# Performance work log

Measured on AMD Instinct MI355X. Metric: run time of the kernel, lower is better.

The kernel has to match this reference:

```python
import jax, jax.numpy as jnp
import numpy as np

N = 50000
E = 800000
F_IN = 96
HID = 128
NCLS = 40
EPS = 0.0  # GINConv default eps


def _mlp(h, W1, b1, W2, b2):
    # Linear -> ReLU -> Linear
    h = jax.nn.relu(h @ W1 + b1)
    return h @ W2 + b2


def _gin_conv(x, edge_index, W1, b1, W2, b2):
    src, dst = edge_index[0], edge_index[1]
    # sum-aggregate neighbor features: scatter-add x[src] into dst
    agg = jax.ops.segment_sum(x[src], dst, num_segments=N)
    return _mlp((1.0 + EPS) * x + agg, W1, b1, W2, b2)


def setup_inputs() -> dict:
    key = jax.random.key(0)
    ks = jax.random.split(key, 12)

    def lin(kw, fan_in, fan_out):
        bound = 1.0 / np.sqrt(fan_in)
        k1, k2 = jax.random.split(kw)
        W = jax.random.uniform(k1, (fan_in, fan_out), jnp.float32, -bound, bound)
        b = jax.random.uniform(k2, (fan_out,), jnp.float32, -bound, bound)
        return W, b

    x = jax.random.normal(ks[0], (N, F_IN), jnp.float32)
    edge_index = jax.random.randint(ks[1], (2, E), 0, N, jnp.int64)
    W1a, b1a = lin(ks[2], F_IN, HID)
    W2a, b2a = lin(ks[3], HID, HID)
    W1b, b1b = lin(ks[4], HID, HID)
    W2b, b2b = lin(ks[5], HID, HID)
    Wfc, bfc = lin(ks[6], HID, NCLS)
    return {"x": x, "edge_index": edge_index,
            "W1a": W1a, "b1a": b1a, "W2a": W2a, "b2a": b2a,
            "W1b": W1b, "b1b": b1b, "W2b": W2b, "b2b": b2b,
            "Wfc": Wfc, "bfc": bfc}


def reference(x, edge_index, W1a, b1a, W2a, b2a, W1b, b1b, W2b, b2b, Wfc, bfc):
    h = _gin_conv(x, edge_index, W1a, b1a, W2a, b2a)
    h = jax.nn.relu(h)
    h = _gin_conv(h, edge_index, W1b, b1b, W2b, b2b)
    return h @ Wfc + bfc  # [N, NCLS]
```

## Files before the change

### kernel.cpp

```cpp
#include <hip/hip_runtime.h>

constexpr int N_NODES = 50000;
constexpr int N_EDGES = 800000;
constexpr int F_INPUT = 96;
constexpr int HID = 128;
constexpr int NCLS = 40;
constexpr int REC = 64;
constexpr int ENT = 62;
constexpr int NBIN = 196;
constexpr int CAPB = 4608;

typedef __attribute__((ext_vector_type(8))) short short8;
typedef __attribute__((ext_vector_type(4))) float f32x4;

__device__ __forceinline__ float bf2f(unsigned int u16) {
    unsigned int x = u16 << 16;
    return __builtin_bit_cast(float, x);
}
__device__ __forceinline__ unsigned short f2bf(float f) {
    unsigned int x = __builtin_bit_cast(unsigned int, f);
    x += 0x7fffu + ((x >> 16) & 1u);
    return (unsigned short)(x >> 16);
}

constexpr int PA_R1 = 391;
constexpr int PA_XC = (N_NODES * F_INPUT / 4 + 255) / 256;
constexpr int PA_F0 = PA_R1 + PA_XC;
constexpr int PA_W1 = PA_F0 + 33;
constexpr int PA_W2 = PA_W1 + 48;
constexpr int PA_W3 = PA_W2 + 64;
constexpr int PA_END = PA_W3 + 64;

__global__ __launch_bounds__(256) void prep_all(
    const float* __restrict__ x,
    const float* __restrict__ W1a, const float* __restrict__ W2a,
    const float* __restrict__ W1b, const float* __restrict__ W2b,
    const float* __restrict__ b2b, const float* __restrict__ Wfc,
    const float* __restrict__ bfc, const int* __restrict__ ei,
    unsigned short* __restrict__ W1aT, unsigned short* __restrict__ W2aT,
    unsigned short* __restrict__ W1bT, unsigned short* __restrict__ WcT,
    float* __restrict__ bc, int* __restrict__ binCursor,
    unsigned int* __restrict__ binBuf, unsigned short* __restrict__ xb) {
    const int b = blockIdx.x;
    const int tid = threadIdx.x;
    if (b < PA_R1) {
        __shared__ int cnt[NBIN];
        __shared__ int base[NBIN];
        for (int i = tid; i < NBIN; i += 256) cnt[i] = 0;
        __syncthreads();
        int binq[8], posq[8];
        unsigned int recq[8];
#pragma unroll
        for (int q = 0; q < 8; ++q) {
            int e = b * 2048 + q * 256 + tid;
            binq[q] = -1;
            if (e < N_EDGES) {
                int src = ei[e], dst = ei[N_EDGES + e];
                int bin = dst >> 8;
                binq[q] = bin;
                recq[q] = (unsigned int)(src & 0xffff) | ((unsigned int)(dst & 255) << 16);
                posq[q] = atomicAdd(&cnt[bin], 1);
            }
        }
        __syncthreads();
        for (int i = tid; i < NBIN; i += 256)
            base[i] = (cnt[i] > 0) ? atomicAdd(&binCursor[i], cnt[i]) : 0;
        __syncthreads();
#pragma unroll
        for (int q = 0; q < 8; ++q) {
            if (binq[q] >= 0) {
                int off = base[binq[q]] + posq[q];
                if (off < CAPB) binBuf[(size_t)binq[q] * CAPB + off] = recq[q];
            }
        }
    } else if (b < PA_F0) {
        int e4 = ((b - PA_R1) * 256 + tid) * 4;
        if (e4 < N_NODES * F_INPUT) {
            float4 v = *reinterpret_cast<const float4*>(&x[e4]);
            uint2 o;
            o.x = (unsigned int)f2bf(v.x) | ((unsigned int)f2bf(v.y) << 16);
            o.y = (unsigned int)f2bf(v.z) | ((unsigned int)f2bf(v.w) << 16);
            *reinterpret_cast<uint2*>(&xb[e4]) = o;
        }
    } else if (b < PA_W1) {
        int idx = (b - PA_F0) * 256 + tid;
        if (idx < 64 * 128) {
            int n = idx >> 7, k = idx & 127;
            float s = 0.f;
            if (n < NCLS) {
                for (int j = 0; j < 128; ++j) s += W2b[k * 128 + j] * Wfc[j * NCLS + n];
            }
            WcT[idx] = f2bf(s);
        } else if (idx < 64 * 128 + 64) {
            int n = idx - 64 * 128;
            float s = 0.f;
            if (n < NCLS) {
                s = bfc[n];
                for (int j = 0; j < 128; ++j) s += b2b[j] * Wfc[j * NCLS + n];
            }
            bc[n] = s;
        }
    } else if (b < PA_W2) {
        int idx = (b - PA_W1) * 256 + tid;
        int n = idx / 96, k = idx % 96;
        W1aT[idx] = f2bf(W1a[k * 128 + n]);
    } else if (b < PA_W3) {
        int idx = (b - PA_W2) * 256 + tid;
        int n = idx >> 7, k = idx & 127;
        W2aT[idx] = f2bf(W2a[k * 128 + n]);
    } else {
        int idx = (b - PA_W3) * 256 + tid;
        int n = idx >> 7, k = idx & 127;
        W1bT[idx] = f2bf(W1b[k * 128 + n]);
    }
}

__global__ __launch_bounds__(1024) void radix2(const int* __restrict__ binCursor,
                                               const unsigned int* __restrict__ binBuf,
                                               unsigned short* __restrict__ bucket) {
    __shared__ int lcnt[256];
    const int bin = blockIdx.x;
    const int tid = threadIdx.x;
    for (int i = tid; i < 256; i += 1024) lcnt[i] = 0;
    __syncthreads();
    int n = binCursor[bin];
    if (n > CAPB) n = CAPB;
    for (int i = tid; i < n; i += 1024) {
        unsigned int r = binBuf[(size_t)bin * CAPB + i];
        int low = (int)(r >> 16);
        int pos = atomicAdd(&lcnt[low], 1);
        if (pos < ENT)
            bucket[(size_t)((bin << 8) + low) * REC + 2 + pos] = (unsigned short)(r & 0xffff);
    }
    __syncthreads();
    for (int i = tid; i < 256; i += 1024) {
        int node = (bin << 8) + i;
        if (node < N_NODES) {
            int c = lcnt[i];
            *reinterpret_cast<int*>(&bucket[(size_t)node * REC]) = (c > ENT ? ENT : c);
        }
    }
}

template<int F>
__global__ __launch_bounds__(256) void gather_bf(const unsigned short* __restrict__ X,
                                                 const unsigned short* __restrict__ bucket,
                                                 unsigned short* __restrict__ OUT) {
    const int wave = threadIdx.x >> 6;
    const int lane = threadIdx.x & 63;
    const int node = blockIdx.x * 4 + wave;
    if (node >= N_NODES) return;
    const unsigned short* rec = &bucket[(size_t)node * REC];
    int deg = *reinterpret_cast<const int*>(rec);
    if (deg > ENT) deg = ENT;

    int v = (lane < deg) ? (int)rec[2 + lane] : 0x7fffffff;
#pragma unroll
    for (int k = 2; k <= 64; k <<= 1) {
#pragma unroll
        for (int j = k >> 1; j > 0; j >>= 1) {
            int pv = __shfl_xor(v, j, 64);
            bool keepmin = (((lane & k) == 0) == ((lane & j) == 0));
            v = keepmin ? (pv < v ? pv : v) : (pv > v ? pv : v);
        }
    }

    const int f = lane * 2;
    const bool act = (f < F);
    float a0 = 0.f, a1 = 0.f;
    int j = 0;
    for (; j + 7 < deg; j += 8) {
        int s[8];
        unsigned int vv[8];
#pragma unroll
        for (int q = 0; q < 8; ++q) s[q] = __shfl(v, j + q, 64);
#pragma unroll
        for (int q = 0; q < 8; ++q) {
            if (act) vv[q] = *reinterpret_cast<const unsigned int*>(&X[(size_t)s[q] * F + f]);
        }
        if (act) {
#pragma unroll
            for (int q = 0; q < 8; ++q) {
                a0 += bf2f(vv[q] & 0xffff);
                a1 += bf2f(vv[q] >> 16);
            }
        }
    }
    if (j + 3 < deg) {
        int s[4];
        unsigned int vv[4];
#pragma unroll
        for (int q = 0; q < 4; ++q) s[q] = __shfl(v, j + q, 64);
#pragma unroll
        for (int q = 0; q < 4; ++q) {
            if (act) vv[q] = *reinterpret_cast<const unsigned int*>(&X[(size_t)s[q] * F + f]);
        }
        if (act) {
#pragma unroll
            for (int q = 0; q < 4; ++q) {
                a0 += bf2f(vv[q] & 0xffff);
                a1 += bf2f(vv[q] >> 16);
            }
        }
        j += 4;
    }
    for (; j < deg; ++j) {
        int s = __shfl(v, j, 64);
        if (act) {
            unsigned int vx = *reinterpret_cast<const unsigned int*>(&X[(size_t)s * F + f]);
            a0 += bf2f(vx & 0xffff);
            a1 += bf2f(vx >> 16);
        }
    }
    if (act) {
        unsigned int xv = *reinterpret_cast<const unsigned int*>(&X[(size_t)node * F + f]);
        a0 += bf2f(xv & 0xffff);
        a1 += bf2f(xv >> 16);
        unsigned int o = (unsigned int)f2bf(a0) | ((unsigned int)f2bf(a1) << 16);
        *reinterpret_cast<unsigned int*>(&OUT[(size_t)node * F + f]) = o;
    }
}

template<int K1, int NT2, int NCOUT, bool RELU2, bool BF16_OUT>
__global__ __launch_bounds__(256) void mlp_fused(const unsigned short* __restrict__ A,
                                                 const unsigned short* __restrict__ W1T,
                                                 const float* __restrict__ b1,
                                                 const unsigned short* __restrict__ W2T,
                                                 const float* __restrict__ b2,
                                                 void* __restrict__ Cout, int M) {
    constexpr int KS1 = K1 / 32;
    constexpr int NT1 = 8;
    constexpr int K2 = 128;
    constexpr int KS2 = K2 / 32;
    __shared__ __align__(16) unsigned short sH[4][16][136];

    const int tid = threadIdx.x;
    const int lane = tid & 63;
    const int wv = tid >> 6;
    const int rowbase = blockIdx.x * 64 + wv * 16;
    const int rA = lane & 15;
    const int kg = lane >> 4;

    int r0 = rowbase + rA;
    if (r0 >= M) r0 = M - 1;
    const unsigned short* ap = A + (size_t)r0 * K1 + kg * 8;
    const unsigned short* b1p = W1T + (size_t)rA * K1 + kg * 8;

    f32x4 acc1[NT1] = {};
#pragma unroll
    for (int ks = 0; ks < KS1; ++ks) {
        short8 a = *reinterpret_cast<const short8*>(ap + ks * 32);
#pragma unroll
        for (int nt = 0; nt < NT1; ++nt) {
            short8 b = *reinterpret_cast<const short8*>(b1p + nt * 16 * K1 + ks * 32);
            acc1[nt] = __builtin_amdgcn_mfma_f32_16x16x32_bf16(a, b, acc1[nt], 0, 0, 0);
        }
    }

    const int oc = lane & 15;
    const int orow = (lane >> 4) * 4;
#pragma unroll
    for (int nt = 0; nt < NT1; ++nt) {
        float bz = b1[nt * 16 + oc];
#pragma unroll
        for (int r = 0; r < 4; ++r) {
            float v = fmaxf(acc1[nt][r] + bz, 0.f);
            sH[wv][orow + r][nt * 16 + oc] = f2bf(v);
        }
    }
    __syncthreads();

    const unsigned short* b2p = W2T + (size_t)rA * K2 + kg * 8;
    f32x4 acc2[NT2] = {};
#pragma unroll
    for (int ks = 0; ks < KS2; ++ks) {
        short8 a = *reinterpret_cast<const short8*>(&sH[wv][rA][kg * 8 + ks * 32]);
#pragma unroll
        for (int nt = 0; nt < NT2; ++nt) {
            short8 b = *reinterpret_cast<const short8*>(b2p + nt * 16 * K2 + ks * 32);
            acc2[nt] = __builtin_amdgcn_mfma_f32_16x16x32_bf16(a, b, acc2[nt], 0, 0, 0);
        }
    }

#pragma unroll
    for (int nt = 0; nt < NT2; ++nt) {
        int col = nt * 16 + oc;
        if (col >= NCOUT) continue;
        float bz = b2[col];
#pragma unroll
        for (int r = 0; r < 4; ++r) {
            int row = rowbase + orow + r;
            if (row < M) {
                float v = acc2[nt][r] + bz;
                if (RELU2) v = fmaxf(v, 0.f);
                if (BF16_OUT)
                    ((unsigned short*)Cout)[(size_t)row * NCOUT + col] = f2bf(v);
                else
                    ((float*)Cout)[(size_t)row * NCOUT + col] = v;
            }
        }
    }
}

extern "C" void kernel_launch(void* const* d_in, const int* in_sizes, int n_in,
                              void* d_out, int out_size, void* d_ws, size_t ws_size,
                              hipStream_t stream) {
    const float* x   = (const float*)d_in[0];
    const int*   ei  = (const int*)d_in[1];
    const float* W1a = (const float*)d_in[2];
    const float* b1a = (const float*)d_in[3];
    const float* W2a = (const float*)d_in[4];
    const float* b2a = (const float*)d_in[5];
    const float* W1b = (const float*)d_in[6];
    const float* b1b = (const float*)d_in[7];
    const float* W2b = (const float*)d_in[8];
    const float* b2b = (const float*)d_in[9];
    const float* Wfc = (const float*)d_in[10];
    const float* bfc = (const float*)d_in[11];
    float* out = (float*)d_out;

    char* p = (char*)d_ws;
    auto alloc = [&](size_t bytes) {
        char* r = p;
        p += (bytes + 255) & ~size_t(255);
        return r;
    };
    unsigned short* xb   = (unsigned short*)alloc((size_t)N_NODES * F_INPUT * 2);
    unsigned short* h0   = (unsigned short*)alloc((size_t)N_NODES * F_INPUT * 2);
    unsigned short* t    = (unsigned short*)alloc((size_t)N_NODES * HID * 2);
    unsigned short* g    = (unsigned short*)alloc((size_t)N_NODES * HID * 2);
    unsigned short* W1aT = (unsigned short*)alloc(128 * 96 * 2);
    unsigned short* W2aT = (unsigned short*)alloc(128 * 128 * 2);
    unsigned short* W1bT = (unsigned short*)alloc(128 * 128 * 2);
    unsigned short* WcT  = (unsigned short*)alloc(64 * 128 * 2);
    float* bc            = (float*)alloc(64 * 4);
    int* binCursor       = (int*)alloc(NBIN * 4);
    unsigned int* binBuf = (unsigned int*)alloc((size_t)NBIN * CAPB * 4);
    unsigned short* bucket = (unsigned short*)alloc((size_t)N_NODES * REC * 2);

    const int nb4 = (N_NODES + 3) / 4;
    const int mb = (N_NODES + 63) / 64;

    hipMemsetAsync(binCursor, 0, NBIN * sizeof(int), stream);

    prep_all<<<PA_END, 256, 0, stream>>>(x, W1a, W2a, W1b, W2b, b2b, Wfc, bfc, ei,
                                         W1aT, W2aT, W1bT, WcT, bc, binCursor, binBuf, xb);

    radix2<<<NBIN, 1024, 0, stream>>>(binCursor, binBuf, bucket);

    gather_bf<F_INPUT><<<nb4, 256, 0, stream>>>(xb, bucket, h0);
    mlp_fused<96, 8, 128, true, true><<<mb, 256, 0, stream>>>(h0, W1aT, b1a, W2aT, b2a, t,
                                                              N_NODES);

    gather_bf<HID><<<nb4, 256, 0, stream>>>(t, bucket, g);
    mlp_fused<128, 4, 40, false, false><<<mb, 256, 0, stream>>>(g, W1bT, b1b, WcT, bc, out,
                                                                N_NODES);
}
```

Before: 232.8 us.

## Fuse neighbor gather-aggregation into the MLP kernel via shared memory

Replaces the separate gather_bf and mlp_fused launches with a single gin_fused kernel. Each wave now aggregates neighbor features for its 16 rows in sequence, writing them into a shared-memory tile that feeds the first MFMA GEMM directly. This removes the h0 and g intermediate buffers, their global writes and reads, and two kernel launches. The cost is less gather parallelism: one wave processes 16 nodes one after another, and far fewer waves are launched, so memory latency may be harder to hide. The now-unneeded block barrier is also dropped, since each wave only touches its own shared rows.

```diff
diff --git a/kernel.cpp b/kernel.cpp
--- a/kernel.cpp
+++ b/kernel.cpp
@@ -142,87 +142,9 @@
     }
 }
 
-template<int F>
-__global__ __launch_bounds__(256) void gather_bf(const unsigned short* __restrict__ X,
+template<int K1, int PADA, int NT2, int NCOUT, bool RELU2, bool BF16_OUT>
+__global__ __launch_bounds__(256) void gin_fused(const unsigned short* __restrict__ X,
                                                  const unsigned short* __restrict__ bucket,
-                                                 unsigned short* __restrict__ OUT) {
-    const int wave = threadIdx.x >> 6;
-    const int lane = threadIdx.x & 63;
-    const int node = blockIdx.x * 4 + wave;
-    if (node >= N_NODES) return;
-    const unsigned short* rec = &bucket[(size_t)node * REC];
-    int deg = *reinterpret_cast<const int*>(rec);
-    if (deg > ENT) deg = ENT;
-
-    int v = (lane < deg) ? (int)rec[2 + lane] : 0x7fffffff;
-#pragma unroll
-    for (int k = 2; k <= 64; k <<= 1) {
-#pragma unroll
-        for (int j = k >> 1; j > 0; j >>= 1) {
-            int pv = __shfl_xor(v, j, 64);
-            bool keepmin = (((lane & k) == 0) == ((lane & j) == 0));
-            v = keepmin ? (pv < v ? pv : v) : (pv > v ? pv : v);
-        }
-    }
-
-    const int f = lane * 2;
-    const bool act = (f < F);
-    float a0 = 0.f, a1 = 0.f;
-    int j = 0;
-    for (; j + 7 < deg; j += 8) {
-        int s[8];
-        unsigned int vv[8];
-#pragma unroll
-        for (int q = 0; q < 8; ++q) s[q] = __shfl(v, j + q, 64);
-#pragma unroll
-        for (int q = 0; q < 8; ++q) {
-            if (act) vv[q] = *reinterpret_cast<const unsigned int*>(&X[(size_t)s[q] * F + f]);
-        }
-        if (act) {
-#pragma unroll
-            for (int q = 0; q < 8; ++q) {
-                a0 += bf2f(vv[q] & 0xffff);
-                a1 += bf2f(vv[q] >> 16);
-            }
-        }
-    }
-    if (j + 3 < deg) {
-        int s[4];
-        unsigned int vv[4];
-#pragma unroll
-        for (int q = 0; q < 4; ++q) s[q] = __shfl(v, j + q, 64);
-#pragma unroll
-        for (int q = 0; q < 4; ++q) {
-            if (act) vv[q] = *reinterpret_cast<const unsigned int*>(&X[(size_t)s[q] * F + f]);
-        }
-        if (act) {
-#pragma unroll
-            for (int q = 0; q < 4; ++q) {
-                a0 += bf2f(vv[q] & 0xffff);
-                a1 += bf2f(vv[q] >> 16);
-            }
-        }
-        j += 4;
-    }
-    for (; j < deg; ++j) {
-        int s = __shfl(v, j, 64);
-        if (act) {
-            unsigned int vx = *reinterpret_cast<const unsigned int*>(&X[(size_t)s * F + f]);
-            a0 += bf2f(vx & 0xffff);
-            a1 += bf2f(vx >> 16);
-        }
-    }
-    if (act) {
-        unsigned int xv = *reinterpret_cast<const unsigned int*>(&X[(size_t)node * F + f]);
-        a0 += bf2f(xv & 0xffff);
-        a1 += bf2f(xv >> 16);
-        unsigned int o = (unsigned int)f2bf(a0) | ((unsigned int)f2bf(a1) << 16);
-        *reinterpret_cast<unsigned int*>(&OUT[(size_t)node * F + f]) = o;
-    }
-}
-
-template<int K1, int NT2, int NCOUT, bool RELU2, bool BF16_OUT>
-__global__ __launch_bounds__(256) void mlp_fused(const unsigned short* __restrict__ A,
                                                  const unsigned short* __restrict__ W1T,
                                                  const float* __restrict__ b1,
                                                  const unsigned short* __restrict__ W2T,
@@ -232,24 +154,94 @@
     constexpr int NT1 = 8;
     constexpr int K2 = 128;
     constexpr int KS2 = K2 / 32;
+    __shared__ __align__(16) unsigned short sA[4][16][PADA];
     __shared__ __align__(16) unsigned short sH[4][16][136];
 
     const int tid = threadIdx.x;
     const int lane = tid & 63;
     const int wv = tid >> 6;
     const int rowbase = blockIdx.x * 64 + wv * 16;
+
+    for (int i = 0; i < 16; ++i) {
+        const int node = rowbase + i;
+        if (node >= M) break;
+        const unsigned short* rec = &bucket[(size_t)node * REC];
+        int deg = *reinterpret_cast<const int*>(rec);
+        if (deg > ENT) deg = ENT;
+        int v = (lane < deg) ? (int)rec[2 + lane] : 0x7fffffff;
+#pragma unroll
+        for (int k = 2; k <= 64; k <<= 1) {
+#pragma unroll
+            for (int j = k >> 1; j > 0; j >>= 1) {
+                int pv = __shfl_xor(v, j, 64);
+                bool keepmin = (((lane & k) == 0) == ((lane & j) == 0));
+                v = keepmin ? (pv < v ? pv : v) : (pv > v ? pv : v);
+            }
+        }
+        const int f = lane * 2;
+        const bool act = (f < K1);
+        float a0 = 0.f, a1 = 0.f;
+        int j = 0;
+        for (; j + 7 < deg; j += 8) {
+            int s[8];
+            unsigned int vv[8];
+#pragma unroll
+            for (int q = 0; q < 8; ++q) s[q] = __shfl(v, j + q, 64);
+#pragma unroll
+            for (int q = 0; q < 8; ++q) {
+                if (act) vv[q] = *reinterpret_cast<const unsigned int*>(&X[(size_t)s[q] * K1 + f]);
+            }
+            if (act) {
+#pragma unroll
+                for (int q = 0; q < 8; ++q) {
+                    a0 += bf2f(vv[q] & 0xffff);
+                    a1 += bf2f(vv[q] >> 16);
+                }
+            }
+        }
+        if (j + 3 < deg) {
+            int s[4];
+            unsigned int vv[4];
+#pragma unroll
+            for (int q = 0; q < 4; ++q) s[q] = __shfl(v, j + q, 64);
+#pragma unroll
+            for (int q = 0; q < 4; ++q) {
+                if (act) vv[q] = *reinterpret_cast<const unsigned int*>(&X[(size_t)s[q] * K1 + f]);
+            }
+            if (act) {
+#pragma unroll
+                for (int q = 0; q < 4; ++q) {
+                    a0 += bf2f(vv[q] & 0xffff);
+                    a1 += bf2f(vv[q] >> 16);
+                }
+            }
+            j += 4;
+        }
+        for (; j < deg; ++j) {
+            int s = __shfl(v, j, 64);
+            if (act) {
+                unsigned int vx = *reinterpret_cast<const unsigned int*>(&X[(size_t)s * K1 + f]);
+                a0 += bf2f(vx & 0xffff);
+                a1 += bf2f(vx >> 16);
+            }
+        }
+        if (act) {
+            unsigned int xv = *reinterpret_cast<const unsigned int*>(&X[(size_t)node * K1 + f]);
+            a0 += bf2f(xv & 0xffff);
+            a1 += bf2f(xv >> 16);
+            unsigned int o = (unsigned int)f2bf(a0) | ((unsigned int)f2bf(a1) << 16);
+            *reinterpret_cast<unsigned int*>(&sA[wv][i][f]) = o;
+        }
+    }
+
     const int rA = lane & 15;
     const int kg = lane >> 4;
-
-    int r0 = rowbase + rA;
-    if (r0 >= M) r0 = M - 1;
-    const unsigned short* ap = A + (size_t)r0 * K1 + kg * 8;
     const unsigned short* b1p = W1T + (size_t)rA * K1 + kg * 8;
 
     f32x4 acc1[NT1] = {};
 #pragma unroll
     for (int ks = 0; ks < KS1; ++ks) {
-        short8 a = *reinterpret_cast<const short8*>(ap + ks * 32);
+        short8 a = *reinterpret_cast<const short8*>(&sA[wv][rA][kg * 8 + ks * 32]);
 #pragma unroll
         for (int nt = 0; nt < NT1; ++nt) {
             short8 b = *reinterpret_cast<const short8*>(b1p + nt * 16 * K1 + ks * 32);
@@ -268,7 +260,6 @@
             sH[wv][orow + r][nt * 16 + oc] = f2bf(v);
         }
     }
-    __syncthreads();
 
     const unsigned short* b2p = W2T + (size_t)rA * K2 + kg * 8;
     f32x4 acc2[NT2] = {};
@@ -326,9 +317,7 @@
         return r;
     };
     unsigned short* xb   = (unsigned short*)alloc((size_t)N_NODES * F_INPUT * 2);
-    unsigned short* h0   = (unsigned short*)alloc((size_t)N_NODES * F_INPUT * 2);
     unsigned short* t    = (unsigned short*)alloc((size_t)N_NODES * HID * 2);
-    unsigned short* g    = (unsigned short*)alloc((size_t)N_NODES * HID * 2);
     unsigned short* W1aT = (unsigned short*)alloc(128 * 96 * 2);
     unsigned short* W2aT = (unsigned short*)alloc(128 * 128 * 2);
     unsigned short* W1bT = (unsigned short*)alloc(128 * 128 * 2);
@@ -338,7 +327,6 @@
     unsigned int* binBuf = (unsigned int*)alloc((size_t)NBIN * CAPB * 4);
     unsigned short* bucket = (unsigned short*)alloc((size_t)N_NODES * REC * 2);
 
-    const int nb4 = (N_NODES + 3) / 4;
     const int mb = (N_NODES + 63) / 64;
 
     hipMemsetAsync(binCursor, 0, NBIN * sizeof(int), stream);
@@ -348,11 +336,9 @@
 
     radix2<<<NBIN, 1024, 0, stream>>>(binCursor, binBuf, bucket);
 
-    gather_bf<F_INPUT><<<nb4, 256, 0, stream>>>(xb, bucket, h0);
-    mlp_fused<96, 8, 128, true, true><<<mb, 256, 0, stream>>>(h0, W1aT, b1a, W2aT, b2a, t,
-                                                              N_NODES);
-
-    gather_bf<HID><<<nb4, 256, 0, stream>>>(t, bucket, g);
-    mlp_fused<128, 4, 40, false, false><<<mb, 256, 0, stream>>>(g, W1bT, b1b, WcT, bc, out,
-                                                                N_NODES);
-}
+    gin_fused<96, 104, 8, 128, true, true><<<mb, 256, 0, stream>>>(
+        xb, bucket, W1aT, b1a, W2aT, b2a, t, N_NODES);
+
+    gin_fused<128, 136, 4, 40, false, false><<<mb, 256, 0, stream>>>(
+        t, bucket, W1bT, b1b, WcT, bc, out, N_NODES);
+}
```

After: 264.5 us. +13.6%, slower.
